# Performance work log

Measured on AMD Instinct MI355X. Metric: run time of the kernel, lower is better.

## Reference

```python
import jax, jax.numpy as jnp
import numpy as np

# config (stands in for global `args` in the original repo)
N = 8192            # args.tRNA + args.disease
NNZ = 262144        # number of edges in adj
N_SEEDS = 256
MASK_DEPTH = 2      # args.maskDepth
KEEP_RATE = 0.9     # args.keepRate


def setup_inputs() -> dict:
    rng = np.random.default_rng(0)
    # duplicate-free edge list (coalesced sparse tensor)
    h = rng.choice(N * N, size=NNZ, replace=False)
    adj_rows = jnp.asarray(h // N, dtype=jnp.int32)
    adj_cols = jnp.asarray(h % N, dtype=jnp.int32)
    key = jax.random.key(0)
    k1, k2, k3 = jax.random.split(key, 3)
    adj_values = jax.random.uniform(k1, (NNZ,), dtype=jnp.float32)
    seeds = jax.random.randint(k2, (N_SEEDS,), 0, N, dtype=jnp.int32)
    complemental = jax.random.uniform(k3, (N, N), dtype=jnp.float32)
    return {"adj_rows": adj_rows, "adj_cols": adj_cols, "adj_values": adj_values,
            "seeds": seeds, "complemental": complemental}


def _forward(adj_rows, adj_cols, adj_values, seeds, complemental):
    rows, cols = adj_rows, adj_cols
    # --- BFS edge masking (sequential per-seed removal == union removal) ---
    keep = jnp.ones((NNZ,), bool)
    seed_mask = jnp.zeros((N,), bool).at[seeds].set(True)
    mask_nodes = seed_mask
    for i in range(MASK_DEPTH):
        incident = keep & (seed_mask[rows] | seed_mask[cols])
        keep = keep & ~incident
        if i != MASK_DEPTH - 1:
            inc_i = incident.astype(jnp.int32)
            nxt = (jnp.zeros((N,), jnp.int32).at[rows].add(inc_i)
                   .at[cols].add(inc_i)) > 0
            seed_mask = nxt
            mask_nodes = mask_nodes | nxt
    # --- random node sampling augments the mask set ---
    key = jax.random.key(42)
    k1, k2, k3 = jax.random.split(key, 3)
    samp_num = int(N * KEEP_RATE)
    samped = jax.random.randint(k1, (samp_num,), 0, N)
    mask_nodes = mask_nodes.at[samped].set(True)
    # --- encoder adj: kept edges, values gathered from complemental, D^-1/2 A D^-1/2 ---
    keep_i = keep.astype(jnp.int32)
    enc_cov = (jnp.zeros((N, N), jnp.int32).at[rows, cols].add(keep_i)) > 0
    enc_dense = jnp.where(enc_cov, complemental, 0.0)
    deg = enc_dense.sum(axis=1)
    norm = (deg + 1e-12) ** -0.5
    enc = enc_dense * norm[:, None] * norm[None, :]
    # --- decoder adj: random mask-node pairs (symmetric) + self loops + kept edges ---
    mask_idx = jnp.nonzero(mask_nodes, size=N, fill_value=0)[0]
    tem_num = mask_nodes.sum()
    u1 = jax.random.uniform(k2, (NNZ,))
    u2 = jax.random.uniform(k3, (NNZ,))
    tem_rows = mask_idx[jnp.floor(u1 * tem_num).astype(jnp.int32)]
    tem_cols = mask_idx[jnp.floor(u2 * tem_num).astype(jnp.int32)]
    ar = jnp.arange(N, dtype=jnp.int32)
    new_rows = jnp.concatenate([tem_rows, tem_cols, ar, rows])
    new_cols = jnp.concatenate([tem_cols, tem_rows, ar, cols])
    valid = jnp.concatenate([jnp.ones((2 * NNZ + N,), jnp.int32), keep_i])
    # hash-dedup in the original == coverage set; values depend only on (r,c)
    dec_cov = (jnp.zeros((N, N), jnp.int32).at[new_rows, new_cols].add(valid)) > 0
    dec = jnp.where(dec_cov, complemental, 0.0)
    return enc, dec


def reference(adj_rows, adj_cols, adj_values, seeds, complemental):
    return _forward(adj_rows, adj_cols, adj_values, seeds, complemental)
```

## Files before the change

kernel.cpp:

```cpp
#include <hip/hip_runtime.h>
#include <stdint.h>
#include <math.h>

typedef float f4 __attribute__((ext_vector_type(4)));

static __device__ __forceinline__ uint32_t rotl32(uint32_t x, int r) {
    return (x << r) | (x >> (32 - r));
}

static __device__ __forceinline__ void tf2x32(uint32_t k0, uint32_t k1,
                                              uint32_t& x0, uint32_t& x1) {
    uint32_t ks2 = k0 ^ k1 ^ 0x1BD11BDAu;
    x0 += k0; x1 += k1;
#define TFR(r) { x0 += x1; x1 = rotl32(x1, r); x1 ^= x0; }
    TFR(13) TFR(15) TFR(26) TFR(6)
    x0 += k1;  x1 += ks2 + 1u;
    TFR(17) TFR(29) TFR(16) TFR(24)
    x0 += ks2; x1 += k0 + 2u;
    TFR(13) TFR(15) TFR(26) TFR(6)
    x0 += k0;  x1 += k1 + 3u;
    TFR(17) TFR(29) TFR(16) TFR(24)
    x0 += k1;  x1 += ks2 + 4u;
    TFR(13) TFR(15) TFR(26) TFR(6)
    x0 += ks2; x1 += k0 + 5u;
#undef TFR
}

struct SubKeys { uint32_t k1a, k1b, k2a, k2b, k3a, k3b; };

static __device__ __forceinline__ SubKeys derive_keys() {
    uint32_t a0 = 0, b0 = 3; tf2x32(0u, 42u, a0, b0);
    uint32_t a1 = 1, b1 = 4; tf2x32(0u, 42u, a1, b1);
    uint32_t a2 = 2, b2 = 5; tf2x32(0u, 42u, a2, b2);
    SubKeys s; s.k1a = a0; s.k1b = a1; s.k2a = a2; s.k2b = b0; s.k3a = b1; s.k3b = b2;
    return s;
}

static __device__ __forceinline__ float bits_to_unit_float(uint32_t b) {
    return __uint_as_float((b >> 9) | 0x3f800000u) - 1.0f;
}

__global__ void k_seed(const int* __restrict__ seeds, int n_seeds,
                       unsigned char* __restrict__ seedm) {
    int i = blockIdx.x * blockDim.x + threadIdx.x;
    if (i < n_seeds) seedm[seeds[i]] = 1;
}

__global__ void k_edge1(const int* __restrict__ rows, const int* __restrict__ cols, int nnz,
                        const unsigned char* __restrict__ seedm,
                        unsigned char* __restrict__ keep, unsigned char* __restrict__ nxt) {
    int e = blockIdx.x * blockDim.x + threadIdx.x;
    if (e >= nnz) return;
    int r = rows[e], c = cols[e];
    bool inc = (seedm[r] | seedm[c]) != 0;
    keep[e] = inc ? 0 : 1;
    if (inc) { nxt[r] = 1; nxt[c] = 1; }
}

__global__ void k_edge2(const int* __restrict__ rows, const int* __restrict__ cols, int nnz,
                        const unsigned char* __restrict__ nxt,
                        unsigned char* __restrict__ keep) {
    int e = blockIdx.x * blockDim.x + threadIdx.x;
    if (e >= nnz) return;
    if (keep[e] && ((nxt[rows[e]] | nxt[cols[e]]) != 0)) keep[e] = 0;
}

__global__ void k_union(int n, const unsigned char* __restrict__ seedm,
                        const unsigned char* __restrict__ nxt,
                        unsigned char* __restrict__ mask) {
    int i = blockIdx.x * blockDim.x + threadIdx.x;
    if (i < n) mask[i] = (unsigned char)(seedm[i] | nxt[i]);
}

__global__ void k_samp(int half, int modmask, unsigned char* __restrict__ mask) {
    int t = blockIdx.x * blockDim.x + threadIdx.x;
    if (t >= half) return;
    SubKeys sk = derive_keys();
    uint32_t x0 = (uint32_t)t, x1 = (uint32_t)(t + half);
    tf2x32(sk.k1a, sk.k1b, x0, x1);
    mask[x0 & (uint32_t)modmask] = 1;
    mask[x1 & (uint32_t)modmask] = 1;
}

__global__ void __launch_bounds__(1024)
k_scan(int n, const unsigned char* __restrict__ mask,
       int* __restrict__ mask_idx, int* __restrict__ tem_num) {
    __shared__ int ssum[1024];
    int t = threadIdx.x;
    int per = n / 1024;
    int base = t * per;
    int loc[8];
    int s = 0;
    for (int j = 0; j < per; ++j) { loc[j] = mask[base + j]; s += loc[j]; }
    ssum[t] = s;
    __syncthreads();
    for (int off = 1; off < 1024; off <<= 1) {
        int v = (t >= off) ? ssum[t - off] : 0;
        __syncthreads();
        ssum[t] += v;
        __syncthreads();
    }
    int excl = ssum[t] - s;
    for (int j = 0; j < per; ++j)
        if (loc[j]) mask_idx[excl++] = base + j;
    if (t == 1023) *tem_num = ssum[1023];
}

__global__ void k_deg(const int* __restrict__ rows, const int* __restrict__ cols, int nnz,
                      const unsigned char* __restrict__ keep,
                      const float* __restrict__ comp, float* __restrict__ deg, int n) {
    int e = blockIdx.x * blockDim.x + threadIdx.x;
    if (e >= nnz) return;
    if (keep[e]) {
        int r = rows[e], c = cols[e];
        atomicAdd(&deg[r], comp[(size_t)r * n + c]);
    }
}

__global__ void k_norm(int n, const float* __restrict__ deg, float* __restrict__ nrm) {
    int i = blockIdx.x * blockDim.x + threadIdx.x;
    if (i < n) nrm[i] = 1.0f / sqrtf(deg[i] + 1e-12f);
}


__global__ void k_cov_encdec(const int* __restrict__ rows, const int* __restrict__ cols,
                             int nnz, int n, const unsigned char* __restrict__ keep,
                             unsigned int* __restrict__ encb, unsigned int* __restrict__ decb) {
    int e = blockIdx.x * blockDim.x + threadIdx.x;
    int wpr = n >> 5;
    if (e < nnz) {
        if (keep[e]) {
            int r = rows[e], c = cols[e];
            size_t w = (size_t)r * wpr + (c >> 5);
            unsigned int b = 1u << (c & 31);
            atomicOr(&encb[w], b);
            atomicOr(&decb[w], b);
        }
    } else if (e < nnz + n) {
        int i = e - nnz;
        atomicOr(&decb[(size_t)i * wpr + (i >> 5)], 1u << (i & 31));
    }
}

__global__ void k_cov_tem(int half, int n, const int* __restrict__ mask_idx,
                          const int* __restrict__ tem_num,
                          unsigned int* __restrict__ decb) {
    int e = blockIdx.x * blockDim.x + threadIdx.x;
    if (e >= half) return;
    SubKeys sk = derive_keys();
    float tf = (float)(*tem_num);
    int wpr = n >> 5;
    uint32_t u1a = (uint32_t)e, u1b = (uint32_t)(e + half);
    tf2x32(sk.k2a, sk.k2b, u1a, u1b);
    uint32_t u2a = (uint32_t)e, u2b = (uint32_t)(e + half);
    tf2x32(sk.k3a, sk.k3b, u2a, u2b);
#pragma unroll
    for (int j = 0; j < 2; ++j) {
        uint32_t b1 = j ? u1b : u1a;
        uint32_t b2 = j ? u2b : u2a;
        float uu1 = bits_to_unit_float(b1);
        float uu2 = bits_to_unit_float(b2);
        int i1 = (int)(uu1 * tf);
        int i2 = (int)(uu2 * tf);
        int r = mask_idx[i1];
        int c = mask_idx[i2];
        atomicOr(&decb[(size_t)r * wpr + (c >> 5)], 1u << (c & 31));
        atomicOr(&decb[(size_t)c * wpr + (r >> 5)], 1u << (r & 31));
    }
}

__global__ void k_dense(int n, const unsigned int* __restrict__ encb,
                        const unsigned int* __restrict__ decb,
                        const float* __restrict__ comp, const float* __restrict__ nrm,
                        float* __restrict__ enc, float* __restrict__ dec) {
    __shared__ unsigned int se[1024], sd[1024];
    int r = blockIdx.x;
    int t = threadIdx.x;
    int wpr = n >> 5;
    se[t] = encb[(size_t)r * wpr + t];
    sd[t] = decb[(size_t)r * wpr + t];
    __syncthreads();
    float nr = nrm[r];
    int sh = (t & 7) * 4;
    int wq = wpr >> 3;
    int wbase = t >> 3;
    size_t rowo = (size_t)r * n;
    const f4* compv = (const f4*)(comp + rowo);
    const f4* nrmv  = (const f4*)nrm;
    f4* encv = (f4*)(enc + rowo);
    f4* decv = (f4*)(dec + rowo);
#pragma unroll
    for (int q = 0; q < 8; ++q) {
        int f = q * wpr + t;
        unsigned int ew = (se[q * wq + wbase] >> sh) & 0xFu;
        unsigned int dw = (sd[q * wq + wbase] >> sh) & 0xFu;
        f4 ev = {0.f, 0.f, 0.f, 0.f};
        f4 dv = {0.f, 0.f, 0.f, 0.f};
        if (ew | dw) {
            f4 cv = compv[f];
            f4 nv = nrmv[f];
            if (ew & 1u) ev.x = cv.x * nr * nv.x;
            if (ew & 2u) ev.y = cv.y * nr * nv.y;
            if (ew & 4u) ev.z = cv.z * nr * nv.z;
            if (ew & 8u) ev.w = cv.w * nr * nv.w;
            if (dw & 1u) dv.x = cv.x;
            if (dw & 2u) dv.y = cv.y;
            if (dw & 4u) dv.z = cv.z;
            if (dw & 8u) dv.w = cv.w;
        }
        __builtin_nontemporal_store(ev, &encv[f]);
        __builtin_nontemporal_store(dv, &decv[f]);
    }
}

__global__ void k_enc(const int* __restrict__ rows, const int* __restrict__ cols, int nnz,
                      const unsigned char* __restrict__ keep,
                      const float* __restrict__ comp, const float* __restrict__ nrm,
                      float* __restrict__ enc, int n) {
    int e = blockIdx.x * blockDim.x + threadIdx.x;
    if (e >= nnz) return;
    if (keep[e]) {
        int r = rows[e], c = cols[e];
        size_t o = (size_t)r * n + c;
        enc[o] = comp[o] * nrm[r] * nrm[c];
    }
}

__global__ void k_dec_base(const int* __restrict__ rows, const int* __restrict__ cols,
                           int nnz, int n, const unsigned char* __restrict__ keep,
                           const float* __restrict__ comp, float* __restrict__ dec) {
    int e = blockIdx.x * blockDim.x + threadIdx.x;
    if (e < nnz) {
        if (keep[e]) {
            size_t o = (size_t)rows[e] * n + cols[e];
            dec[o] = comp[o];
        }
    } else if (e < nnz + n) {
        int i = e - nnz;
        size_t o = (size_t)i * n + i;
        dec[o] = comp[o];
    }
}

__global__ void k_dec_tem(int half, int n, const int* __restrict__ mask_idx,
                          const int* __restrict__ tem_num,
                          const float* __restrict__ comp, float* __restrict__ dec) {
    int e = blockIdx.x * blockDim.x + threadIdx.x;
    if (e >= half) return;
    SubKeys sk = derive_keys();
    float tf = (float)(*tem_num);
    uint32_t u1a = (uint32_t)e, u1b = (uint32_t)(e + half);
    tf2x32(sk.k2a, sk.k2b, u1a, u1b);
    uint32_t u2a = (uint32_t)e, u2b = (uint32_t)(e + half);
    tf2x32(sk.k3a, sk.k3b, u2a, u2b);
#pragma unroll
    for (int j = 0; j < 2; ++j) {
        uint32_t b1 = j ? u1b : u1a;
        uint32_t b2 = j ? u2b : u2a;
        float uu1 = bits_to_unit_float(b1);
        float uu2 = bits_to_unit_float(b2);
        int i1 = (int)(uu1 * tf);
        int i2 = (int)(uu2 * tf);
        int r = mask_idx[i1];
        int c = mask_idx[i2];
        size_t o1 = (size_t)r * n + c;
        size_t o2 = (size_t)c * n + r;
        dec[o1] = comp[o1];
        dec[o2] = comp[o2];
    }
}

extern "C" void kernel_launch(void* const* d_in, const int* in_sizes, int n_in,
                              void* d_out, int out_size, void* d_ws, size_t ws_size,
                              hipStream_t stream) {
    const int*   rows  = (const int*)d_in[0];
    const int*   cols  = (const int*)d_in[1];
    const int*   seeds = (const int*)d_in[3];
    const float* comp  = (const float*)d_in[4];

    const int nnz     = in_sizes[0];
    const int n_seeds = in_sizes[3];
    const int n       = (int)(sqrt((double)in_sizes[4]) + 0.5);

    float* enc = (float*)d_out;
    float* dec = enc + (size_t)n * n;

    char* ws = (char*)d_ws;
    float* deg            = (float*)(ws);
    float* nrm            = (float*)(ws + 4 * (size_t)n);
    int*   mask_idx       = (int*)  (ws + 8 * (size_t)n);
    int*   tem_num        = (int*)  (ws + 12 * (size_t)n + 256 - 256);
    unsigned char* seedm  = (unsigned char*)(ws + 12 * (size_t)n + 256);
    unsigned char* nxt    = seedm + n;
    unsigned char* mask   = nxt + n;
    unsigned char* keep   = mask + n;

    size_t small_end = 12 * (size_t)n + 256 + 3 * (size_t)n + (size_t)nnz;
    size_t bm_off    = (small_end + 255) & ~(size_t)255;
    size_t bm_bytes  = ((size_t)n * (size_t)n) / 8;
    bool fast = (ws_size >= bm_off + 2 * bm_bytes) && ((n & 1023) == 0) && (n >> 5) <= 1024;

    const int B = 256;
    int samp_num = (int)((double)n * 0.9);
    int shalf = samp_num / 2;
    int ehalf = nnz / 2;

    if (fast) {
        unsigned int* encb = (unsigned int*)(ws + bm_off);
        unsigned int* decb = (unsigned int*)(ws + bm_off + bm_bytes);

        hipMemsetAsync(d_ws, 0, bm_off + 2 * bm_bytes, stream);

        k_seed <<<(n_seeds + B - 1) / B, B, 0, stream>>>(seeds, n_seeds, seedm);
        k_edge1<<<(nnz + B - 1) / B, B, 0, stream>>>(rows, cols, nnz, seedm, keep, nxt);
        k_edge2<<<(nnz + B - 1) / B, B, 0, stream>>>(rows, cols, nnz, nxt, keep);
        k_union<<<(n + B - 1) / B, B, 0, stream>>>(n, seedm, nxt, mask);
        k_samp <<<(shalf + B - 1) / B, B, 0, stream>>>(shalf, n - 1, mask);
        k_scan <<<1, 1024, 0, stream>>>(n, mask, mask_idx, tem_num);
        k_deg  <<<(nnz + B - 1) / B, B, 0, stream>>>(rows, cols, nnz, keep, comp, deg, n);
        k_norm <<<(n + B - 1) / B, B, 0, stream>>>(n, deg, nrm);

        k_cov_encdec<<<(nnz + n + B - 1) / B, B, 0, stream>>>(rows, cols, nnz, n, keep, encb, decb);
        k_cov_tem   <<<(ehalf + B - 1) / B, B, 0, stream>>>(ehalf, n, mask_idx, tem_num, decb);

        k_dense<<<n, n >> 5, 0, stream>>>(n, encb, decb, comp, nrm, enc, dec);
    } else {
        size_t zbytes = 12 * (size_t)n + 256 + 3 * (size_t)n;
        hipMemsetAsync(d_ws, 0, zbytes, stream);
        hipMemsetAsync(d_out, 0, (size_t)out_size * sizeof(float), stream);

        k_seed <<<(n_seeds + B - 1) / B, B, 0, stream>>>(seeds, n_seeds, seedm);
        k_edge1<<<(nnz + B - 1) / B, B, 0, stream>>>(rows, cols, nnz, seedm, keep, nxt);
        k_edge2<<<(nnz + B - 1) / B, B, 0, stream>>>(rows, cols, nnz, nxt, keep);
        k_union<<<(n + B - 1) / B, B, 0, stream>>>(n, seedm, nxt, mask);
        k_samp <<<(shalf + B - 1) / B, B, 0, stream>>>(shalf, n - 1, mask);
        k_scan <<<1, 1024, 0, stream>>>(n, mask, mask_idx, tem_num);
        k_deg  <<<(nnz + B - 1) / B, B, 0, stream>>>(rows, cols, nnz, keep, comp, deg, n);
        k_norm <<<(n + B - 1) / B, B, 0, stream>>>(n, deg, nrm);
        k_enc  <<<(nnz + B - 1) / B, B, 0, stream>>>(rows, cols, nnz, keep, comp, nrm, enc, n);
        k_dec_base<<<(nnz + n + B - 1) / B, B, 0, stream>>>(rows, cols, nnz, n, keep, comp, dec);
        k_dec_tem<<<(ehalf + B - 1) / B, B, 0, stream>>>(ehalf, n, mask_idx, tem_num, comp, dec);
    }
}
```

Measured before the change: 737.3 us.

## Replace global coverage bitmaps with per-row CSR buckets built in LDS

Drops the two n×n global bitmaps (16 MB memset plus global atomics) and instead builds CSR-style per-row column lists for kept edges and random decoder pairs via count, scan and fill kernels. The dense kernel then rebuilds each row's coverage bitmap in shared memory with LDS atomics before writing enc and dec. This removes the large memset and the scattered global atomicOr traffic, at the cost of more kernel launches, recomputing the random pairs twice, and restricting the fast path to n==8192. It also skips loading nrm when no encoder bit is set in a group.

```diff
diff --git a/kernel.cpp b/kernel.cpp
--- a/kernel.cpp
+++ b/kernel.cpp
@@ -38,6 +38,23 @@
 
 static __device__ __forceinline__ float bits_to_unit_float(uint32_t b) {
     return __uint_as_float((b >> 9) | 0x3f800000u) - 1.0f;
+}
+
+struct TemPair { int r, c; };
+static __device__ __forceinline__ void tem_pairs(int e, int half, float tf,
+                                                 const int* __restrict__ mask_idx,
+                                                 const SubKeys& sk,
+                                                 TemPair& p0, TemPair& p1) {
+    uint32_t u1a = (uint32_t)e, u1b = (uint32_t)(e + half);
+    tf2x32(sk.k2a, sk.k2b, u1a, u1b);
+    uint32_t u2a = (uint32_t)e, u2b = (uint32_t)(e + half);
+    tf2x32(sk.k3a, sk.k3b, u2a, u2b);
+    float a1 = bits_to_unit_float(u1a), a2 = bits_to_unit_float(u2a);
+    float b1 = bits_to_unit_float(u1b), b2 = bits_to_unit_float(u2b);
+    p0.r = mask_idx[(int)(a1 * tf)];
+    p0.c = mask_idx[(int)(a2 * tf)];
+    p1.r = mask_idx[(int)(b1 * tf)];
+    p1.c = mask_idx[(int)(b2 * tf)];
 }
 
 __global__ void k_seed(const int* __restrict__ seeds, int n_seeds,
@@ -123,90 +140,131 @@
 }
 
 
-__global__ void k_cov_encdec(const int* __restrict__ rows, const int* __restrict__ cols,
-                             int nnz, int n, const unsigned char* __restrict__ keep,
-                             unsigned int* __restrict__ encb, unsigned int* __restrict__ decb) {
-    int e = blockIdx.x * blockDim.x + threadIdx.x;
-    int wpr = n >> 5;
-    if (e < nnz) {
-        if (keep[e]) {
-            int r = rows[e], c = cols[e];
-            size_t w = (size_t)r * wpr + (c >> 5);
-            unsigned int b = 1u << (c & 31);
-            atomicOr(&encb[w], b);
-            atomicOr(&decb[w], b);
-        }
-    } else if (e < nnz + n) {
-        int i = e - nnz;
-        atomicOr(&decb[(size_t)i * wpr + (i >> 5)], 1u << (i & 31));
-    }
-}
-
-__global__ void k_cov_tem(int half, int n, const int* __restrict__ mask_idx,
-                          const int* __restrict__ tem_num,
-                          unsigned int* __restrict__ decb) {
+__global__ void k_cnt_kept(const int* __restrict__ rows, int nnz,
+                           const unsigned char* __restrict__ keep,
+                           int* __restrict__ cnt_k) {
+    int e = blockIdx.x * blockDim.x + threadIdx.x;
+    if (e < nnz && keep[e]) atomicAdd(&cnt_k[rows[e]], 1);
+}
+
+__global__ void k_fill_kept(const int* __restrict__ rows, const int* __restrict__ cols,
+                            int nnz, const unsigned char* __restrict__ keep,
+                            int* __restrict__ cur_k, unsigned short* __restrict__ cols_k) {
+    int e = blockIdx.x * blockDim.x + threadIdx.x;
+    if (e < nnz && keep[e]) {
+        int p = atomicAdd(&cur_k[rows[e]], 1);
+        cols_k[p] = (unsigned short)cols[e];
+    }
+}
+
+__global__ void k_cnt_tem(int half, const int* __restrict__ mask_idx,
+                          const int* __restrict__ tem_num, int* __restrict__ cnt_t) {
     int e = blockIdx.x * blockDim.x + threadIdx.x;
     if (e >= half) return;
     SubKeys sk = derive_keys();
     float tf = (float)(*tem_num);
-    int wpr = n >> 5;
-    uint32_t u1a = (uint32_t)e, u1b = (uint32_t)(e + half);
-    tf2x32(sk.k2a, sk.k2b, u1a, u1b);
-    uint32_t u2a = (uint32_t)e, u2b = (uint32_t)(e + half);
-    tf2x32(sk.k3a, sk.k3b, u2a, u2b);
-#pragma unroll
-    for (int j = 0; j < 2; ++j) {
-        uint32_t b1 = j ? u1b : u1a;
-        uint32_t b2 = j ? u2b : u2a;
-        float uu1 = bits_to_unit_float(b1);
-        float uu2 = bits_to_unit_float(b2);
-        int i1 = (int)(uu1 * tf);
-        int i2 = (int)(uu2 * tf);
-        int r = mask_idx[i1];
-        int c = mask_idx[i2];
-        atomicOr(&decb[(size_t)r * wpr + (c >> 5)], 1u << (c & 31));
-        atomicOr(&decb[(size_t)c * wpr + (r >> 5)], 1u << (r & 31));
-    }
-}
-
-__global__ void k_dense(int n, const unsigned int* __restrict__ encb,
-                        const unsigned int* __restrict__ decb,
-                        const float* __restrict__ comp, const float* __restrict__ nrm,
-                        float* __restrict__ enc, float* __restrict__ dec) {
-    __shared__ unsigned int se[1024], sd[1024];
+    TemPair p0, p1;
+    tem_pairs(e, half, tf, mask_idx, sk, p0, p1);
+    atomicAdd(&cnt_t[p0.r], 1); atomicAdd(&cnt_t[p0.c], 1);
+    atomicAdd(&cnt_t[p1.r], 1); atomicAdd(&cnt_t[p1.c], 1);
+}
+
+__global__ void k_fill_tem(int half, const int* __restrict__ mask_idx,
+                           const int* __restrict__ tem_num,
+                           int* __restrict__ cur_t, unsigned short* __restrict__ cols_t) {
+    int e = blockIdx.x * blockDim.x + threadIdx.x;
+    if (e >= half) return;
+    SubKeys sk = derive_keys();
+    float tf = (float)(*tem_num);
+    TemPair p0, p1;
+    tem_pairs(e, half, tf, mask_idx, sk, p0, p1);
+    int p;
+    p = atomicAdd(&cur_t[p0.r], 1); cols_t[p] = (unsigned short)p0.c;
+    p = atomicAdd(&cur_t[p0.c], 1); cols_t[p] = (unsigned short)p0.r;
+    p = atomicAdd(&cur_t[p1.r], 1); cols_t[p] = (unsigned short)p1.c;
+    p = atomicAdd(&cur_t[p1.c], 1); cols_t[p] = (unsigned short)p1.r;
+}
+
+__global__ void __launch_bounds__(1024)
+k_scan_off(int n, const int* __restrict__ cnt_k, int* __restrict__ off_k, int* __restrict__ cur_k,
+           const int* __restrict__ cnt_t, int* __restrict__ off_t, int* __restrict__ cur_t) {
+    __shared__ int ssum[1024];
+    const int* cnt = blockIdx.x ? cnt_t : cnt_k;
+    int* off = blockIdx.x ? off_t : off_k;
+    int* cur = blockIdx.x ? cur_t : cur_k;
+    int t = threadIdx.x;
+    int per = n / 1024;
+    int base = t * per;
+    int loc[8];
+    int s = 0;
+    for (int j = 0; j < per; ++j) { loc[j] = cnt[base + j]; s += loc[j]; }
+    ssum[t] = s;
+    __syncthreads();
+    for (int o = 1; o < 1024; o <<= 1) {
+        int v = (t >= o) ? ssum[t - o] : 0;
+        __syncthreads();
+        ssum[t] += v;
+        __syncthreads();
+    }
+    int run = ssum[t] - s;
+    for (int j = 0; j < per; ++j) { off[base + j] = run; cur[base + j] = run; run += loc[j]; }
+}
+
+__global__ void __launch_bounds__(256)
+k_dense_lds(int n,
+            const int* __restrict__ off_k, const int* __restrict__ cnt_k,
+            const unsigned short* __restrict__ cols_k,
+            const int* __restrict__ off_t, const int* __restrict__ cnt_t,
+            const unsigned short* __restrict__ cols_t,
+            const float* __restrict__ comp, const float* __restrict__ nrm,
+            float* __restrict__ enc, float* __restrict__ dec) {
+    __shared__ unsigned int se[256], sd[256];
     int r = blockIdx.x;
     int t = threadIdx.x;
-    int wpr = n >> 5;
-    se[t] = encb[(size_t)r * wpr + t];
-    sd[t] = decb[(size_t)r * wpr + t];
+    se[t] = 0; sd[t] = 0;
+    __syncthreads();
+    int ok = off_k[r], ck = cnt_k[r];
+    for (int i = t; i < ck; i += 256) {
+        int c = cols_k[ok + i];
+        unsigned int b = 1u << (c & 31);
+        atomicOr(&se[c >> 5], b);
+        atomicOr(&sd[c >> 5], b);
+    }
+    int ot = off_t[r], ct = cnt_t[r];
+    for (int i = t; i < ct; i += 256) {
+        int c = cols_t[ot + i];
+        atomicOr(&sd[c >> 5], 1u << (c & 31));
+    }
+    if (t == 0) atomicOr(&sd[r >> 5], 1u << (r & 31));
     __syncthreads();
     float nr = nrm[r];
-    int sh = (t & 7) * 4;
-    int wq = wpr >> 3;
-    int wbase = t >> 3;
     size_t rowo = (size_t)r * n;
     const f4* compv = (const f4*)(comp + rowo);
     const f4* nrmv  = (const f4*)nrm;
     f4* encv = (f4*)(enc + rowo);
     f4* decv = (f4*)(dec + rowo);
+    int sh = (t & 7) * 4;
+    int wb = t >> 3;
 #pragma unroll
     for (int q = 0; q < 8; ++q) {
-        int f = q * wpr + t;
-        unsigned int ew = (se[q * wq + wbase] >> sh) & 0xFu;
-        unsigned int dw = (sd[q * wq + wbase] >> sh) & 0xFu;
+        int f = q * 256 + t;
+        unsigned int ew = (se[q * 32 + wb] >> sh) & 0xFu;
+        unsigned int dw = (sd[q * 32 + wb] >> sh) & 0xFu;
         f4 ev = {0.f, 0.f, 0.f, 0.f};
         f4 dv = {0.f, 0.f, 0.f, 0.f};
         if (ew | dw) {
             f4 cv = compv[f];
-            f4 nv = nrmv[f];
-            if (ew & 1u) ev.x = cv.x * nr * nv.x;
-            if (ew & 2u) ev.y = cv.y * nr * nv.y;
-            if (ew & 4u) ev.z = cv.z * nr * nv.z;
-            if (ew & 8u) ev.w = cv.w * nr * nv.w;
             if (dw & 1u) dv.x = cv.x;
             if (dw & 2u) dv.y = cv.y;
             if (dw & 4u) dv.z = cv.z;
             if (dw & 8u) dv.w = cv.w;
+            if (ew) {
+                f4 nv = nrmv[f];
+                if (ew & 1u) ev.x = cv.x * nr * nv.x;
+                if (ew & 2u) ev.y = cv.y * nr * nv.y;
+                if (ew & 4u) ev.z = cv.z * nr * nv.z;
+                if (ew & 8u) ev.w = cv.w * nr * nv.w;
+            }
         }
         __builtin_nontemporal_store(ev, &encv[f]);
         __builtin_nontemporal_store(dv, &decv[f]);
@@ -249,25 +307,13 @@
     if (e >= half) return;
     SubKeys sk = derive_keys();
     float tf = (float)(*tem_num);
-    uint32_t u1a = (uint32_t)e, u1b = (uint32_t)(e + half);
-    tf2x32(sk.k2a, sk.k2b, u1a, u1b);
-    uint32_t u2a = (uint32_t)e, u2b = (uint32_t)(e + half);
-    tf2x32(sk.k3a, sk.k3b, u2a, u2b);
-#pragma unroll
-    for (int j = 0; j < 2; ++j) {
-        uint32_t b1 = j ? u1b : u1a;
-        uint32_t b2 = j ? u2b : u2a;
-        float uu1 = bits_to_unit_float(b1);
-        float uu2 = bits_to_unit_float(b2);
-        int i1 = (int)(uu1 * tf);
-        int i2 = (int)(uu2 * tf);
-        int r = mask_idx[i1];
-        int c = mask_idx[i2];
-        size_t o1 = (size_t)r * n + c;
-        size_t o2 = (size_t)c * n + r;
-        dec[o1] = comp[o1];
-        dec[o2] = comp[o2];
-    }
+    TemPair p0, p1;
+    tem_pairs(e, half, tf, mask_idx, sk, p0, p1);
+    size_t o;
+    o = (size_t)p0.r * n + p0.c; dec[o] = comp[o];
+    o = (size_t)p0.c * n + p0.r; dec[o] = comp[o];
+    o = (size_t)p1.r * n + p1.c; dec[o] = comp[o];
+    o = (size_t)p1.c * n + p1.r; dec[o] = comp[o];
 }
 
 extern "C" void kernel_launch(void* const* d_in, const int* in_sizes, int n_in,
@@ -289,16 +335,17 @@
     float* deg            = (float*)(ws);
     float* nrm            = (float*)(ws + 4 * (size_t)n);
     int*   mask_idx       = (int*)  (ws + 8 * (size_t)n);
-    int*   tem_num        = (int*)  (ws + 12 * (size_t)n + 256 - 256);
+    int*   tem_num        = (int*)  (ws + 12 * (size_t)n);
     unsigned char* seedm  = (unsigned char*)(ws + 12 * (size_t)n + 256);
     unsigned char* nxt    = seedm + n;
     unsigned char* mask   = nxt + n;
     unsigned char* keep   = mask + n;
 
     size_t small_end = 12 * (size_t)n + 256 + 3 * (size_t)n + (size_t)nnz;
-    size_t bm_off    = (small_end + 255) & ~(size_t)255;
-    size_t bm_bytes  = ((size_t)n * (size_t)n) / 8;
-    bool fast = (ws_size >= bm_off + 2 * bm_bytes) && ((n & 1023) == 0) && (n >> 5) <= 1024;
+    size_t bko = (small_end + 255) & ~(size_t)255;
+
+    size_t bucket_end = bko + 24 * (size_t)n + 6 * (size_t)nnz;
+    bool fast = (ws_size >= bucket_end) && (n == 8192);
 
     const int B = 256;
     int samp_num = (int)((double)n * 0.9);
@@ -306,10 +353,16 @@
     int ehalf = nnz / 2;
 
     if (fast) {
-        unsigned int* encb = (unsigned int*)(ws + bm_off);
-        unsigned int* decb = (unsigned int*)(ws + bm_off + bm_bytes);
-
-        hipMemsetAsync(d_ws, 0, bm_off + 2 * bm_bytes, stream);
+        int* cnt_k = (int*)(ws + bko);
+        int* cnt_t = (int*)(ws + bko + 4 * (size_t)n);
+        int* off_k = (int*)(ws + bko + 8 * (size_t)n);
+        int* cur_k = (int*)(ws + bko + 12 * (size_t)n);
+        int* off_t = (int*)(ws + bko + 16 * (size_t)n);
+        int* cur_t = (int*)(ws + bko + 20 * (size_t)n);
+        unsigned short* cols_k = (unsigned short*)(ws + bko + 24 * (size_t)n);
+        unsigned short* cols_t = cols_k + (size_t)nnz;
+
+        hipMemsetAsync(d_ws, 0, bko + 8 * (size_t)n, stream);
 
         k_seed <<<(n_seeds + B - 1) / B, B, 0, stream>>>(seeds, n_seeds, seedm);
         k_edge1<<<(nnz + B - 1) / B, B, 0, stream>>>(rows, cols, nnz, seedm, keep, nxt);
@@ -320,14 +373,19 @@
         k_deg  <<<(nnz + B - 1) / B, B, 0, stream>>>(rows, cols, nnz, keep, comp, deg, n);
         k_norm <<<(n + B - 1) / B, B, 0, stream>>>(n, deg, nrm);
 
-        k_cov_encdec<<<(nnz + n + B - 1) / B, B, 0, stream>>>(rows, cols, nnz, n, keep, encb, decb);
-        k_cov_tem   <<<(ehalf + B - 1) / B, B, 0, stream>>>(ehalf, n, mask_idx, tem_num, decb);
-
-        k_dense<<<n, n >> 5, 0, stream>>>(n, encb, decb, comp, nrm, enc, dec);
+        k_cnt_kept<<<(nnz + B - 1) / B, B, 0, stream>>>(rows, nnz, keep, cnt_k);
+        k_cnt_tem <<<(ehalf + B - 1) / B, B, 0, stream>>>(ehalf, mask_idx, tem_num, cnt_t);
+        k_scan_off<<<2, 1024, 0, stream>>>(n, cnt_k, off_k, cur_k, cnt_t, off_t, cur_t);
+        k_fill_kept<<<(nnz + B - 1) / B, B, 0, stream>>>(rows, cols, nnz, keep, cur_k, cols_k);
+        k_fill_tem <<<(ehalf + B - 1) / B, B, 0, stream>>>(ehalf, mask_idx, tem_num, cur_t, cols_t);
+
+        k_dense_lds<<<n, 256, 0, stream>>>(n, off_k, cnt_k, cols_k,
+                                           off_t, cnt_t, cols_t,
+                                           comp, nrm, enc, dec);
     } else {
         size_t zbytes = 12 * (size_t)n + 256 + 3 * (size_t)n;
         hipMemsetAsync(d_ws, 0, zbytes, stream);
-        hipMemsetAsync(d_out, 0, (size_t)out_size * sizeof(float), stream);
+        hipMemsetAsync(d_out, 0, 2 * (size_t)n * (size_t)n * sizeof(float), stream);
 
         k_seed <<<(n_seeds + B - 1) / B, B, 0, stream>>>(seeds, n_seeds, seedm);
         k_edge1<<<(nnz + B - 1) / B, B, 0, stream>>>(rows, cols, nnz, seedm, keep, nxt);
```

New measurement: 796.0 us. +8.0%, slower.

## Build coverage bitmaps per 32-row window in shared memory inside dense kernel

Applied to the files above, without the earlier changes.

Replaces the global coverage-bitmap kernels and the global memset with a single kernel where each block owns 32 rows. The block builds enc/dec bitmaps in LDS by scanning all edges and regenerating all random pairs, then writes its dense rows. This removes the global bitmap memset, the global atomics and one bitmap round trip. In exchange every block rescans the whole edge list and recomputes the Threefry values, so that redundant work grows with the number of blocks (256). Occupancy is also limited by about 80KB of LDS per block.

```diff
diff --git a/kernel.cpp b/kernel.cpp
--- a/kernel.cpp
+++ b/kernel.cpp
@@ -122,94 +122,108 @@
     if (i < n) nrm[i] = 1.0f / sqrtf(deg[i] + 1e-12f);
 }
 
-
-__global__ void k_cov_encdec(const int* __restrict__ rows, const int* __restrict__ cols,
-                             int nnz, int n, const unsigned char* __restrict__ keep,
-                             unsigned int* __restrict__ encb, unsigned int* __restrict__ decb) {
-    int e = blockIdx.x * blockDim.x + threadIdx.x;
-    int wpr = n >> 5;
-    if (e < nnz) {
-        if (keep[e]) {
-            int r = rows[e], c = cols[e];
-            size_t w = (size_t)r * wpr + (c >> 5);
+#define DG 32
+
+__global__ void __launch_bounds__(512)
+k_dense_win(const int* __restrict__ rows, const int* __restrict__ cols,
+            int nnz, int ehalf, int n,
+            const unsigned char* __restrict__ keep,
+            const int* __restrict__ mask_idx, const int* __restrict__ tem_num,
+            const float* __restrict__ comp, const float* __restrict__ nrm,
+            float* __restrict__ enc, float* __restrict__ dec) {
+    __shared__ unsigned int sbm[16384];
+    __shared__ unsigned short smi[8192];
+    const int t = threadIdx.x;
+    const int base = blockIdx.x * DG;
+    const int wpr = n >> 5;
+
+    for (int i = t; i < 16384; i += 512) sbm[i] = 0;
+    for (int i = t; i < n; i += 512) smi[i] = (unsigned short)mask_idx[i];
+    __syncthreads();
+
+    for (int e = t; e < nnz; e += 512) {
+        if (!keep[e]) continue;
+        int r = rows[e];
+        unsigned int rr = (unsigned int)(r - base);
+        if (rr < DG) {
+            int c = cols[e];
             unsigned int b = 1u << (c & 31);
-            atomicOr(&encb[w], b);
-            atomicOr(&decb[w], b);
-        }
-    } else if (e < nnz + n) {
-        int i = e - nnz;
-        atomicOr(&decb[(size_t)i * wpr + (i >> 5)], 1u << (i & 31));
-    }
-}
-
-__global__ void k_cov_tem(int half, int n, const int* __restrict__ mask_idx,
-                          const int* __restrict__ tem_num,
-                          unsigned int* __restrict__ decb) {
-    int e = blockIdx.x * blockDim.x + threadIdx.x;
-    if (e >= half) return;
-    SubKeys sk = derive_keys();
-    float tf = (float)(*tem_num);
-    int wpr = n >> 5;
-    uint32_t u1a = (uint32_t)e, u1b = (uint32_t)(e + half);
-    tf2x32(sk.k2a, sk.k2b, u1a, u1b);
-    uint32_t u2a = (uint32_t)e, u2b = (uint32_t)(e + half);
-    tf2x32(sk.k3a, sk.k3b, u2a, u2b);
+            atomicOr(&sbm[rr * wpr + (c >> 5)], b);
+            atomicOr(&sbm[8192 + rr * wpr + (c >> 5)], b);
+        }
+    }
+    if (t < DG) {
+        int c = base + t;
+        atomicOr(&sbm[8192 + t * wpr + (c >> 5)], 1u << (c & 31));
+    }
+    __syncthreads();
+
+    for (int i = 0; i < DG; ++i) {
+        int r = base + i;
+        float nr = nrm[r];
+        size_t rowo = (size_t)r * n;
+        const f4* compv = (const f4*)(comp + rowo);
+        const f4* nrmv  = (const f4*)nrm;
+        f4* encv = (f4*)(enc + rowo);
+#pragma unroll 4
+        for (int f = t; f < (n >> 2); f += 512) {
+            unsigned int ew = (sbm[i * wpr + (f >> 3)] >> ((f & 7) * 4)) & 0xFu;
+            f4 ev = {0.f, 0.f, 0.f, 0.f};
+            if (ew) {
+                f4 cv = compv[f];
+                f4 nv = nrmv[f];
+                if (ew & 1u) ev.x = cv.x * nr * nv.x;
+                if (ew & 2u) ev.y = cv.y * nr * nv.y;
+                if (ew & 4u) ev.z = cv.z * nr * nv.z;
+                if (ew & 8u) ev.w = cv.w * nr * nv.w;
+            }
+            __builtin_nontemporal_store(ev, &encv[f]);
+        }
+    }
+
+    {
+        SubKeys sk = derive_keys();
+        float tf = (float)(*tem_num);
+        for (int e = t; e < ehalf; e += 512) {
+            uint32_t u1a = (uint32_t)e, u1b = (uint32_t)(e + ehalf);
+            tf2x32(sk.k2a, sk.k2b, u1a, u1b);
+            uint32_t u2a = (uint32_t)e, u2b = (uint32_t)(e + ehalf);
+            tf2x32(sk.k3a, sk.k3b, u2a, u2b);
 #pragma unroll
-    for (int j = 0; j < 2; ++j) {
-        uint32_t b1 = j ? u1b : u1a;
-        uint32_t b2 = j ? u2b : u2a;
-        float uu1 = bits_to_unit_float(b1);
-        float uu2 = bits_to_unit_float(b2);
-        int i1 = (int)(uu1 * tf);
-        int i2 = (int)(uu2 * tf);
-        int r = mask_idx[i1];
-        int c = mask_idx[i2];
-        atomicOr(&decb[(size_t)r * wpr + (c >> 5)], 1u << (c & 31));
-        atomicOr(&decb[(size_t)c * wpr + (r >> 5)], 1u << (r & 31));
-    }
-}
-
-__global__ void k_dense(int n, const unsigned int* __restrict__ encb,
-                        const unsigned int* __restrict__ decb,
-                        const float* __restrict__ comp, const float* __restrict__ nrm,
-                        float* __restrict__ enc, float* __restrict__ dec) {
-    __shared__ unsigned int se[1024], sd[1024];
-    int r = blockIdx.x;
-    int t = threadIdx.x;
-    int wpr = n >> 5;
-    se[t] = encb[(size_t)r * wpr + t];
-    sd[t] = decb[(size_t)r * wpr + t];
+            for (int j = 0; j < 2; ++j) {
+                uint32_t b1 = j ? u1b : u1a;
+                uint32_t b2 = j ? u2b : u2a;
+                int i1 = (int)(bits_to_unit_float(b1) * tf);
+                int i2 = (int)(bits_to_unit_float(b2) * tf);
+                int r = smi[i1];
+                int c = smi[i2];
+                unsigned int rr = (unsigned int)(r - base);
+                unsigned int cc = (unsigned int)(c - base);
+                if (rr < DG) atomicOr(&sbm[8192 + rr * wpr + (c >> 5)], 1u << (c & 31));
+                if (cc < DG) atomicOr(&sbm[8192 + cc * wpr + (r >> 5)], 1u << (r & 31));
+            }
+        }
+    }
     __syncthreads();
-    float nr = nrm[r];
-    int sh = (t & 7) * 4;
-    int wq = wpr >> 3;
-    int wbase = t >> 3;
-    size_t rowo = (size_t)r * n;
-    const f4* compv = (const f4*)(comp + rowo);
-    const f4* nrmv  = (const f4*)nrm;
-    f4* encv = (f4*)(enc + rowo);
-    f4* decv = (f4*)(dec + rowo);
-#pragma unroll
-    for (int q = 0; q < 8; ++q) {
-        int f = q * wpr + t;
-        unsigned int ew = (se[q * wq + wbase] >> sh) & 0xFu;
-        unsigned int dw = (sd[q * wq + wbase] >> sh) & 0xFu;
-        f4 ev = {0.f, 0.f, 0.f, 0.f};
-        f4 dv = {0.f, 0.f, 0.f, 0.f};
-        if (ew | dw) {
-            f4 cv = compv[f];
-            f4 nv = nrmv[f];
-            if (ew & 1u) ev.x = cv.x * nr * nv.x;
-            if (ew & 2u) ev.y = cv.y * nr * nv.y;
-            if (ew & 4u) ev.z = cv.z * nr * nv.z;
-            if (ew & 8u) ev.w = cv.w * nr * nv.w;
-            if (dw & 1u) dv.x = cv.x;
-            if (dw & 2u) dv.y = cv.y;
-            if (dw & 4u) dv.z = cv.z;
-            if (dw & 8u) dv.w = cv.w;
-        }
-        __builtin_nontemporal_store(ev, &encv[f]);
-        __builtin_nontemporal_store(dv, &decv[f]);
+
+    for (int i = 0; i < DG; ++i) {
+        int r = base + i;
+        size_t rowo = (size_t)r * n;
+        const f4* compv = (const f4*)(comp + rowo);
+        f4* decv = (f4*)(dec + rowo);
+#pragma unroll 4
+        for (int f = t; f < (n >> 2); f += 512) {
+            unsigned int dw = (sbm[8192 + i * wpr + (f >> 3)] >> ((f & 7) * 4)) & 0xFu;
+            f4 dv = {0.f, 0.f, 0.f, 0.f};
+            if (dw) {
+                f4 cv = compv[f];
+                if (dw & 1u) dv.x = cv.x;
+                if (dw & 2u) dv.y = cv.y;
+                if (dw & 4u) dv.z = cv.z;
+                if (dw & 8u) dv.w = cv.w;
+            }
+            __builtin_nontemporal_store(dv, &decv[f]);
+        }
     }
 }
 
@@ -257,10 +271,8 @@
     for (int j = 0; j < 2; ++j) {
         uint32_t b1 = j ? u1b : u1a;
         uint32_t b2 = j ? u2b : u2a;
-        float uu1 = bits_to_unit_float(b1);
-        float uu2 = bits_to_unit_float(b2);
-        int i1 = (int)(uu1 * tf);
-        int i2 = (int)(uu2 * tf);
+        int i1 = (int)(bits_to_unit_float(b1) * tf);
+        int i2 = (int)(bits_to_unit_float(b2) * tf);
         int r = mask_idx[i1];
         int c = mask_idx[i2];
         size_t o1 = (size_t)r * n + c;
@@ -289,54 +301,35 @@
     float* deg            = (float*)(ws);
     float* nrm            = (float*)(ws + 4 * (size_t)n);
     int*   mask_idx       = (int*)  (ws + 8 * (size_t)n);
-    int*   tem_num        = (int*)  (ws + 12 * (size_t)n + 256 - 256);
+    int*   tem_num        = (int*)  (ws + 12 * (size_t)n);
     unsigned char* seedm  = (unsigned char*)(ws + 12 * (size_t)n + 256);
     unsigned char* nxt    = seedm + n;
     unsigned char* mask   = nxt + n;
     unsigned char* keep   = mask + n;
 
-    size_t small_end = 12 * (size_t)n + 256 + 3 * (size_t)n + (size_t)nnz;
-    size_t bm_off    = (small_end + 255) & ~(size_t)255;
-    size_t bm_bytes  = ((size_t)n * (size_t)n) / 8;
-    bool fast = (ws_size >= bm_off + 2 * bm_bytes) && ((n & 1023) == 0) && (n >> 5) <= 1024;
-
     const int B = 256;
     int samp_num = (int)((double)n * 0.9);
     int shalf = samp_num / 2;
     int ehalf = nnz / 2;
 
-    if (fast) {
-        unsigned int* encb = (unsigned int*)(ws + bm_off);
-        unsigned int* decb = (unsigned int*)(ws + bm_off + bm_bytes);
-
-        hipMemsetAsync(d_ws, 0, bm_off + 2 * bm_bytes, stream);
-
-        k_seed <<<(n_seeds + B - 1) / B, B, 0, stream>>>(seeds, n_seeds, seedm);
-        k_edge1<<<(nnz + B - 1) / B, B, 0, stream>>>(rows, cols, nnz, seedm, keep, nxt);
-        k_edge2<<<(nnz + B - 1) / B, B, 0, stream>>>(rows, cols, nnz, nxt, keep);
-        k_union<<<(n + B - 1) / B, B, 0, stream>>>(n, seedm, nxt, mask);
-        k_samp <<<(shalf + B - 1) / B, B, 0, stream>>>(shalf, n - 1, mask);
-        k_scan <<<1, 1024, 0, stream>>>(n, mask, mask_idx, tem_num);
-        k_deg  <<<(nnz + B - 1) / B, B, 0, stream>>>(rows, cols, nnz, keep, comp, deg, n);
-        k_norm <<<(n + B - 1) / B, B, 0, stream>>>(n, deg, nrm);
-
-        k_cov_encdec<<<(nnz + n + B - 1) / B, B, 0, stream>>>(rows, cols, nnz, n, keep, encb, decb);
-        k_cov_tem   <<<(ehalf + B - 1) / B, B, 0, stream>>>(ehalf, n, mask_idx, tem_num, decb);
-
-        k_dense<<<n, n >> 5, 0, stream>>>(n, encb, decb, comp, nrm, enc, dec);
+    size_t zbytes = 12 * (size_t)n + 256 + 3 * (size_t)n;
+    hipMemsetAsync(d_ws, 0, zbytes, stream);
+
+    k_seed <<<(n_seeds + B - 1) / B, B, 0, stream>>>(seeds, n_seeds, seedm);
+    k_edge1<<<(nnz + B - 1) / B, B, 0, stream>>>(rows, cols, nnz, seedm, keep, nxt);
+    k_edge2<<<(nnz + B - 1) / B, B, 0, stream>>>(rows, cols, nnz, nxt, keep);
+    k_union<<<(n + B - 1) / B, B, 0, stream>>>(n, seedm, nxt, mask);
+    k_samp <<<(shalf + B - 1) / B, B, 0, stream>>>(shalf, n - 1, mask);
+    k_scan <<<1, 1024, 0, stream>>>(n, mask, mask_idx, tem_num);
+    k_deg  <<<(nnz + B - 1) / B, B, 0, stream>>>(rows, cols, nnz, keep, comp, deg, n);
+    k_norm <<<(n + B - 1) / B, B, 0, stream>>>(n, deg, nrm);
+
+    if (n == 8192) {
+        k_dense_win<<<n / DG, 512, 0, stream>>>(rows, cols, nnz, ehalf, n,
+                                                keep, mask_idx, tem_num,
+                                                comp, nrm, enc, dec);
     } else {
-        size_t zbytes = 12 * (size_t)n + 256 + 3 * (size_t)n;
-        hipMemsetAsync(d_ws, 0, zbytes, stream);
-        hipMemsetAsync(d_out, 0, (size_t)out_size * sizeof(float), stream);
-
-        k_seed <<<(n_seeds + B - 1) / B, B, 0, stream>>>(seeds, n_seeds, seedm);
-        k_edge1<<<(nnz + B - 1) / B, B, 0, stream>>>(rows, cols, nnz, seedm, keep, nxt);
-        k_edge2<<<(nnz + B - 1) / B, B, 0, stream>>>(rows, cols, nnz, nxt, keep);
-        k_union<<<(n + B - 1) / B, B, 0, stream>>>(n, seedm, nxt, mask);
-        k_samp <<<(shalf + B - 1) / B, B, 0, stream>>>(shalf, n - 1, mask);
-        k_scan <<<1, 1024, 0, stream>>>(n, mask, mask_idx, tem_num);
-        k_deg  <<<(nnz + B - 1) / B, B, 0, stream>>>(rows, cols, nnz, keep, comp, deg, n);
-        k_norm <<<(n + B - 1) / B, B, 0, stream>>>(n, deg, nrm);
+        hipMemsetAsync(d_out, 0, 2 * (size_t)n * (size_t)n * sizeof(float), stream);
         k_enc  <<<(nnz + B - 1) / B, B, 0, stream>>>(rows, cols, nnz, keep, comp, nrm, enc, n);
         k_dec_base<<<(nnz + n + B - 1) / B, B, 0, stream>>>(rows, cols, nnz, n, keep, comp, dec);
         k_dec_tem<<<(ehalf + B - 1) / B, B, 0, stream>>>(ehalf, n, mask_idx, tem_num, comp, dec);
```

After: 1.131 ms. +53.4%, slower.
